# Performance work log

Hardware: AMD Instinct MI355X
Metric: run time of the kernel (lower is better)

Reference implementation:

```python
import jax, jax.numpy as jnp
import numpy as np

N, E, F_IN, F_HID, F_OUT, B = 50000, 800000, 128, 128, 128, 64
EPS = 1e-5


def _sage_conv(x, src, dst, w_l, b_l, w_r):
    # PyG SAGEConv (mean aggr): out = lin_l(mean_{j in N(i)} x_j) + lin_r(x_i)
    msg_sum = jax.ops.segment_sum(x[src], dst, num_segments=N)          # [N, F]
    deg = jax.ops.segment_sum(jnp.ones((src.shape[0],), x.dtype), dst, num_segments=N)
    agg = msg_sum / jnp.clip(deg, 1.0)[:, None]
    return agg @ w_l + b_l + x @ w_r


def _batch_norm(x, gamma, beta):
    # PyG BatchNorm (training): biased batch stats over the node dimension
    mu = jnp.mean(x, axis=0)
    var = jnp.mean((x - mu) ** 2, axis=0)
    return (x - mu) * jax.lax.rsqrt(var + EPS) * gamma + beta


def setup_inputs() -> dict:
    key = jax.random.key(0)
    ks = jax.random.split(key, 12)
    x = jax.random.normal(ks[0], (N, F_IN), jnp.float32)
    edge_index = jax.random.randint(ks[1], (2, E), 0, N, jnp.int64 if jax.config.jax_enable_x64 else jnp.int32)
    batch = jnp.sort(jax.random.randint(ks[2], (N,), 0, B))
    s1 = 1.0 / np.sqrt(F_IN)
    s2 = 1.0 / np.sqrt(F_HID)
    return {
        "x": x, "edge_index": edge_index, "batch": batch,
        "w_l1": jax.random.uniform(ks[3], (F_IN, F_HID), jnp.float32, -s1, s1),
        "b_l1": jax.random.uniform(ks[4], (F_HID,), jnp.float32, -s1, s1),
        "w_r1": jax.random.uniform(ks[5], (F_IN, F_HID), jnp.float32, -s1, s1),
        "g1": jnp.ones((F_HID,), jnp.float32),
        "beta1": jnp.zeros((F_HID,), jnp.float32),
        "w_l2": jax.random.uniform(ks[6], (F_HID, F_OUT), jnp.float32, -s2, s2),
        "b_l2": jax.random.uniform(ks[7], (F_OUT,), jnp.float32, -s2, s2),
        "w_r2": jax.random.uniform(ks[8], (F_HID, F_OUT), jnp.float32, -s2, s2),
        "g2": jnp.ones((F_OUT,), jnp.float32),
        "beta2": jnp.zeros((F_OUT,), jnp.float32),
    }


def reference(x, edge_index, batch, w_l1, b_l1, w_r1, g1, beta1, w_l2, b_l2, w_r2, g2, beta2):
    src, dst = edge_index[0], edge_index[1]
    h = jax.nn.relu(_batch_norm(_sage_conv(x, src, dst, w_l1, b_l1, w_r1), g1, beta1))
    h = jax.nn.relu(_batch_norm(_sage_conv(h, src, dst, w_l2, b_l2, w_r2), g2, beta2))
    # global_mean_pool over graph ids
    pooled = jax.ops.segment_sum(h, batch, num_segments=B)              # [B, F_OUT]
    cnt = jax.ops.segment_sum(jnp.ones((N,), h.dtype), batch, num_segments=B)
    return pooled / jnp.clip(cnt, 1.0)[:, None]
```

## Files before the change

### kernel.cpp

```cpp
#include <hip/hip_runtime.h>
#include <hip/hip_bf16.h>
#include <stdint.h>

typedef unsigned int uint32;
typedef unsigned short ushort16;

typedef __attribute__((ext_vector_type(8))) short short8;
typedef __attribute__((ext_vector_type(4))) float f32x4;

#define N_NODES 50000
#define N_EDGES 800000
#define FD      128
#define NGRAPH  64
#define MTILES  3125
#define NBK     196
#define GB      391
#define GB2     782
#define PCH     32
#define KCH     98

__device__ __forceinline__ float bf2f(ushort16 u){
  union { uint32 i; float f; } v; v.i = ((uint32)u) << 16; return v.f;
}
__device__ __forceinline__ float bf2f_lo(uint32 w){ union{uint32 i;float f;}v; v.i = w << 16; return v.f; }
__device__ __forceinline__ float bf2f_hi(uint32 w){ union{uint32 i;float f;}v; v.i = w & 0xffff0000u; return v.f; }
__device__ __forceinline__ ushort16 f2bf(float f){
  uint32 u = __float_as_uint(f);
  u += 0x7fffu + ((u >> 16) & 1u);
  return (ushort16)(u >> 16);
}

__device__ __forceinline__ int ld_idx(const void* p, uint32 is64, size_t i){
  return is64 ? (int)((const long long*)p)[i] : ((const int*)p)[i];
}
__device__ __forceinline__ float ld_f(const void* p, uint32 isf32, int i){
  return isf32 ? ((const float*)p)[i] : bf2f(((const ushort16*)p)[i]);
}

__device__ __forceinline__ void get_flags(const uint32* __restrict__ xw,
    const uint32* __restrict__ eiw, uint32& isf32, uint32& is64)
{
  int l = threadIdx.x & 63;
  uint32 w = xw[l];
  uint32 e8 = (w >> 7) & 0xFFu;
  bool bf_like = (e8 >= 0x70u && e8 <= 0x82u);
  unsigned long long m = __ballot(bf_like);
  isf32 = (__popcll(m) < 32) ? 1u : 0u;
  uint32 hi = (l < 8) ? eiw[2*l + 1] : 1u;
  unsigned long long z = __ballot(hi == 0u);
  is64 = ((z & 0xFFull) == 0xFFull) ? 1u : 0u;
}


__global__ __launch_bounds__(256) void pack_gseg_prep_kernel(
    const void* __restrict__ ei, const void* __restrict__ batch,
    const void* __restrict__ X,
    const void* __restrict__ WL1, const void* __restrict__ WR1,
    const void* __restrict__ WL2, const void* __restrict__ WR2,
    uint32* __restrict__ pack0, uint32* __restrict__ hist, uint32* __restrict__ gstart,
    ushort16* __restrict__ xb, short* __restrict__ wfrag)
{
  uint32 isf32, is64;
  get_flags((const uint32*)X, (const uint32*)ei, isf32, is64);
  int tid = threadIdx.x;
  if (blockIdx.x < GB){
    __shared__ uint32 h[256];
    h[tid] = 0u;
    __syncthreads();
    int base = blockIdx.x*2048;
    for (int r = 0; r < 8; ++r){
      int i = base + r*256 + tid;
      if (i < N_EDGES){
        uint32 s = (uint32)ld_idx(ei, is64, i);
        uint32 d = (uint32)ld_idx(ei, is64, (size_t)N_EDGES + i);
        pack0[i] = (d << 16) | s;
        atomicAdd(&h[d >> 8], 1u);
      }
    }
    __syncthreads();
    hist[blockIdx.x*256 + tid] = h[tid];
  } else if (blockIdx.x < GB + 196){
    int t = (blockIdx.x - GB)*256 + tid;
    if (t >= N_NODES) return;
    int b1 = ld_idx(batch, is64, t);
    int b0 = (t == 0) ? -1 : ld_idx(batch, is64, t - 1);
    for (int g = b0 + 1; g <= b1; ++g) gstart[g] = (uint32)t;
    if (t == N_NODES - 1)
      for (int g = b1 + 1; g <= NGRAPH; ++g) gstart[g] = (uint32)N_NODES;
  } else if (blockIdx.x < GB + 196 + 3125){
    if (!isf32) return;
    size_t e = ((size_t)(blockIdx.x - GB - 196)*256 + tid)*8;
    const float* p = (const float*)X + e;
    float4 u = *(const float4*)p;
    float4 v = *(const float4*)(p + 4);
    uint4 o;
    o.x = (uint32)f2bf(u.x) | ((uint32)f2bf(u.y) << 16);
    o.y = (uint32)f2bf(u.z) | ((uint32)f2bf(u.w) << 16);
    o.z = (uint32)f2bf(v.x) | ((uint32)f2bf(v.y) << 16);
    o.w = (uint32)f2bf(v.z) | ((uint32)f2bf(v.w) << 16);
    *(uint4*)(xb + e) = o;
  } else {
    int t = (blockIdx.x - GB - 196 - 3125)*256 + tid;
    int layer = t >> 15;
    int r = t & 32767;
    int k = r >> 7, n = r & 127;
    const void* w = layer ? (k < 128 ? WL2 : WR2) : (k < 128 ? WL1 : WR1);
    int kk = k & 127;
    float wv = ld_f(w, isf32, kk*128 + n);
    int off = (((k >> 5)*8 + (n >> 4))*64 + (n & 15) + 16*((kk >> 3) & 3))*8 + (kk & 7);
    wfrag[layer*32768 + off] = (short)f2bf(wv);
  }
}

__global__ __launch_bounds__(1024) void scan_hist_kernel(const uint32* __restrict__ hist,
    uint32* __restrict__ off, uint32* __restrict__ bbase)
{
  __shared__ uint32 part[4][256];
  __shared__ uint32 lds[256];
  __shared__ uint32 bb[256];
  int tid = threadIdx.x;
  int seg = tid >> 8, b = tid & 255;
  int k0 = seg*KCH, k1 = (k0 + KCH < GB) ? k0 + KCH : GB;
  uint32 sum = 0;
  for (int k = k0; k < k1; ++k) sum += hist[k*256 + b];
  part[seg][b] = sum;
  __syncthreads();
  uint32 tot = 0, x = 0;
  if (seg == 0){
    tot = part[0][b] + part[1][b] + part[2][b] + part[3][b];
    x = tot; lds[b] = x;
  }
  __syncthreads();
  for (int o = 1; o < 256; o <<= 1){
    uint32 y = 0;
    if (seg == 0 && b >= o) y = lds[b - o];
    __syncthreads();
    if (seg == 0){ x += y; lds[b] = x; }
    __syncthreads();
  }
  if (seg == 0){
    uint32 base = x - tot;
    bb[b] = base;
    if (b <= NBK) bbase[b] = (b < NBK) ? base : (uint32)N_EDGES;
  }
  __syncthreads();
  uint32 run = bb[b];
  for (int s = 0; s < seg; ++s) run += part[s][b];
  for (int k = k0; k < k1; ++k){
    off[k*256 + b] = run;
    run += hist[k*256 + b];
  }
}

__global__ __launch_bounds__(256) void scatter_kernel(const uint32* __restrict__ pack0,
    const uint32* __restrict__ off, uint32* __restrict__ pack1)
{
  __shared__ uint32 cur[256];
  int tid = threadIdx.x;
  cur[tid] = off[blockIdx.x*256 + tid];
  __syncthreads();
  int base = blockIdx.x*2048;
  for (int r = 0; r < 8; ++r){
    int i = base + r*256 + tid;
    if (i < N_EDGES){
      uint32 p = pack0[i];
      uint32 pos = atomicAdd(&cur[p >> 24], 1u);
      pack1[pos] = p;
    }
  }
}

__global__ __launch_bounds__(256) void bucket_csr_kernel(const uint32* __restrict__ pack1,
    const uint32* __restrict__ bbase, uint32* __restrict__ rowstart,
    uint32* __restrict__ deg, ushort16* __restrict__ colidx)
{
  __shared__ uint32 cnt[256];
  __shared__ uint32 lds[256];
  __shared__ uint32 cur[256];
  int tid = threadIdx.x;
  int bk = blockIdx.x;
  uint32 e0 = bbase[bk], e1 = bbase[bk + 1];
  cnt[tid] = 0u;
  __syncthreads();
  for (uint32 i = e0 + tid; i < e1; i += 256)
    atomicAdd(&cnt[(pack1[i] >> 16) & 255u], 1u);
  __syncthreads();
  uint32 v = cnt[tid];
  uint32 x = v;
  lds[tid] = x; __syncthreads();
  for (int o = 1; o < 256; o <<= 1){
    uint32 y = (tid >= o) ? lds[tid - o] : 0u;
    __syncthreads();
    x += y; lds[tid] = x;
    __syncthreads();
  }
  uint32 start = e0 + x - v;
  int node = bk*256 + tid;
  if (node < N_NODES){ rowstart[node] = start; deg[node] = v; }
  cur[tid] = start;
  __syncthreads();
  for (uint32 i = e0 + tid; i < e1; i += 256){
    uint32 p = pack1[i];
    uint32 pos = atomicAdd(&cur[(p >> 16) & 255u], 1u);
    colidx[pos] = (ushort16)(p & 0xFFFFu);
  }
}


__device__ __forceinline__ void acc8(float* a, uint4 v, const float* s0, const float* h0, int APPLY){
  float f[8];
  f[0] = bf2f_lo(v.x); f[1] = bf2f_hi(v.x);
  f[2] = bf2f_lo(v.y); f[3] = bf2f_hi(v.y);
  f[4] = bf2f_lo(v.z); f[5] = bf2f_hi(v.z);
  f[6] = bf2f_lo(v.w); f[7] = bf2f_hi(v.w);
#pragma unroll
  for (int j = 0; j < 8; ++j)
    a[j] += APPLY ? fmaxf(f[j]*s0[j] + h0[j], 0.f) : f[j];
}

template<int APPLY>
__global__ __launch_bounds__(256) void agg_kernel(const ushort16* __restrict__ Xd,
    const void* __restrict__ Xraw, const void* __restrict__ eiraw,
    const uint32* __restrict__ rowstart, const uint32* __restrict__ deg,
    const ushort16* __restrict__ colidx,
    const float* __restrict__ sc, const float* __restrict__ sh,
    ushort16* __restrict__ out)
{
  uint32 isf32, is64;
  get_flags((const uint32*)Xraw, (const uint32*)eiraw, isf32, is64);
  const ushort16* X = (APPLY == 0 && !isf32) ? (const ushort16*)Xraw : Xd;
  int t = blockIdx.x*256 + threadIdx.x;
  int node = t >> 4;
  int l = t & 15;
  uint32 st = rowstart[node];
  uint32 d  = deg[node];
  float s0[8], h0[8];
#pragma unroll
  for (int j = 0; j < 8; ++j){
    s0[j] = APPLY ? sc[l*8 + j] : 0.f;
    h0[j] = APPLY ? sh[l*8 + j] : 0.f;
  }
  float a[8];
#pragma unroll
  for (int j = 0; j < 8; ++j) a[j] = 0.f;
  const ushort16* Xl = X + l*8;
  uint32 i = 0;
  for (; i < d && ((st + i) & 3u); ++i){
    uint32 c = colidx[st + i];
    acc8(a, *(const uint4*)(Xl + (size_t)c*FD), s0, h0, APPLY);
  }
  for (; i + 8 <= d; i += 8){
    uint2 cA = *(const uint2*)(colidx + st + i);
    uint2 cB = *(const uint2*)(colidx + st + i + 4);
    uint4 v0 = *(const uint4*)(Xl + (size_t)(cA.x & 0xFFFFu)*FD);
    uint4 v1 = *(const uint4*)(Xl + (size_t)(cA.x >> 16)*FD);
    uint4 v2 = *(const uint4*)(Xl + (size_t)(cA.y & 0xFFFFu)*FD);
    uint4 v3 = *(const uint4*)(Xl + (size_t)(cA.y >> 16)*FD);
    uint4 v4 = *(const uint4*)(Xl + (size_t)(cB.x & 0xFFFFu)*FD);
    uint4 v5 = *(const uint4*)(Xl + (size_t)(cB.x >> 16)*FD);
    uint4 v6 = *(const uint4*)(Xl + (size_t)(cB.y & 0xFFFFu)*FD);
    uint4 v7 = *(const uint4*)(Xl + (size_t)(cB.y >> 16)*FD);
    acc8(a, v0, s0, h0, APPLY); acc8(a, v1, s0, h0, APPLY);
    acc8(a, v2, s0, h0, APPLY); acc8(a, v3, s0, h0, APPLY);
    acc8(a, v4, s0, h0, APPLY); acc8(a, v5, s0, h0, APPLY);
    acc8(a, v6, s0, h0, APPLY); acc8(a, v7, s0, h0, APPLY);
  }
  for (; i + 4 <= d; i += 4){
    uint2 cA = *(const uint2*)(colidx + st + i);
    uint4 v0 = *(const uint4*)(Xl + (size_t)(cA.x & 0xFFFFu)*FD);
    uint4 v1 = *(const uint4*)(Xl + (size_t)(cA.x >> 16)*FD);
    uint4 v2 = *(const uint4*)(Xl + (size_t)(cA.y & 0xFFFFu)*FD);
    uint4 v3 = *(const uint4*)(Xl + (size_t)(cA.y >> 16)*FD);
    acc8(a, v0, s0, h0, APPLY); acc8(a, v1, s0, h0, APPLY);
    acc8(a, v2, s0, h0, APPLY); acc8(a, v3, s0, h0, APPLY);
  }
  for (; i < d; ++i){
    uint32 c = colidx[st + i];
    acc8(a, *(const uint4*)(Xl + (size_t)c*FD), s0, h0, APPLY);
  }
  float inv = 1.f / fmaxf((float)d, 1.f);
  uint4 o;
  o.x = (uint32)f2bf(a[0]*inv) | ((uint32)f2bf(a[1]*inv) << 16);
  o.y = (uint32)f2bf(a[2]*inv) | ((uint32)f2bf(a[3]*inv) << 16);
  o.z = (uint32)f2bf(a[4]*inv) | ((uint32)f2bf(a[5]*inv) << 16);
  o.w = (uint32)f2bf(a[6]*inv) | ((uint32)f2bf(a[7]*inv) << 16);
  *(uint4*)(out + (size_t)node*FD + l*8) = o;
}


__device__ __forceinline__ short8 affine_relu8(short8 a, const float* sc, const float* sh, int koff){
  short8 r;
#pragma unroll
  for (int j = 0; j < 8; ++j){
    float v = bf2f((ushort16)a[j]) * sc[koff + j] + sh[koff + j];
    r[j] = (short)f2bf(fmaxf(v, 0.f));
  }
  return r;
}

template<int APPLY>
__global__ __launch_bounds__(256) void gemm_bn_kernel(
    const ushort16* __restrict__ A0, const ushort16* __restrict__ A1d,
    const void* __restrict__ A1raw, const void* __restrict__ eiraw,
    const short* __restrict__ wfrag, const void* __restrict__ bias,
    const float* __restrict__ sc, const float* __restrict__ sh,
    const void* __restrict__ Xraw,
    ushort16* __restrict__ hpre, float* __restrict__ bnpart)
{
  __shared__ float red[256];
  uint32 isf32, is64;
  get_flags((const uint32*)Xraw, (const uint32*)eiraw, isf32, is64);
  const ushort16* A1 = (A1raw && !isf32) ? (const ushort16*)A1raw : A1d;
  int tid = threadIdx.x;
  red[tid] = 0.f;
  int wave = tid >> 6, lane = tid & 63, lq = lane >> 4, lm = lane & 15;
  int mt = blockIdx.x*4 + wave;
  bool valid = mt < MTILES;
  size_t m0 = (size_t)((valid ? mt : 0)*16 + lm);
  f32x4 acc[8];
#pragma unroll
  for (int i = 0; i < 8; ++i) acc[i] = (f32x4){0.f,0.f,0.f,0.f};

#pragma unroll
  for (int ks = 0; ks < 8; ++ks){
    int koff = (ks & 3)*32 + lq*8;
    const short* srcp = (const short*)(ks < 4 ? A0 : A1);
    short8 a = *(const short8*)(srcp + m0*FD + koff);
    if (APPLY && ks >= 4) a = affine_relu8(a, sc, sh, koff);
#pragma unroll
    for (int nt = 0; nt < 8; ++nt){
      short8 b = *(const short8*)&wfrag[((ks*8 + nt)*64 + lane)*8];
      acc[nt] = __builtin_amdgcn_mfma_f32_16x16x32_bf16(a, b, acc[nt], 0, 0, 0);
    }
  }

  __syncthreads();
#pragma unroll
  for (int nt = 0; nt < 8; ++nt){
    int colc = nt*16 + lm;
    float bb = ld_f(bias, isf32, colc);
    float s = 0.f, s2 = 0.f;
    if (valid){
      size_t nb = (size_t)mt*16 + lq*4;
#pragma unroll
      for (int r = 0; r < 4; ++r){
        float val = acc[nt][r] + bb;
        hpre[(nb + r)*FD + colc] = f2bf(val);
        s += val; s2 += val*val;
      }
    }
    s  += __shfl_xor(s, 16);  s  += __shfl_xor(s, 32);
    s2 += __shfl_xor(s2, 16); s2 += __shfl_xor(s2, 32);
    if (lq == 0){
      atomicAdd(&red[colc], s);
      atomicAdd(&red[128 + colc], s2);
    }
  }
  __syncthreads();
  bnpart[blockIdx.x*256 + tid] = red[tid];
}


__global__ __launch_bounds__(256) void bn_final_kernel(const float* __restrict__ bnpart,
    const void* __restrict__ gamma, const void* __restrict__ beta,
    const void* __restrict__ Xraw, const void* __restrict__ eiraw,
    float* __restrict__ scale, float* __restrict__ shift)
{
  uint32 isf32, is64;
  get_flags((const uint32*)Xraw, (const uint32*)eiraw, isf32, is64);
  int tid = threadIdx.x;
  int f = blockIdx.x*8 + (tid >> 5);
  int l = tid & 31;
  float s = 0.f, q = 0.f;
  for (int b = l; b < GB2; b += 32){
    s += bnpart[b*256 + f];
    q += bnpart[b*256 + 128 + f];
  }
#pragma unroll
  for (int m = 16; m >= 1; m >>= 1){
    s += __shfl_xor(s, m);
    q += __shfl_xor(q, m);
  }
  if (l == 0){
    const float invN = 1.0f / (float)N_NODES;
    float mu  = s * invN;
    float var = q * invN - mu*mu;
    float scv = ld_f(gamma, isf32, f) * rsqrtf(var + 1e-5f);
    scale[f] = scv;
    shift[f] = ld_f(beta, isf32, f) - mu * scv;
  }
}


__global__ __launch_bounds__(256) void pool_partial_kernel(const ushort16* __restrict__ hp,
    const float* __restrict__ scale, const float* __restrict__ shift,
    const uint32* __restrict__ gstart, float* __restrict__ pool_part)
{
  __shared__ float wred[4*16*8];
  int tid = threadIdx.x;
  int g = blockIdx.x >> 5, chunk = blockIdx.x & 31;
  int slot = tid >> 4, l = tid & 15;
  int wave = tid >> 6, lane = tid & 63;
  uint32 st = gstart[g], cnt = gstart[g+1] - st;
  uint32 per = (cnt + PCH - 1) >> 5;
  uint32 b0 = st + chunk*per;
  uint32 b1 = b0 + per;
  uint32 e1 = st + cnt;
  if (b1 > e1) b1 = e1;
  float s0[8], h0[8], a[8];
#pragma unroll
  for (int j = 0; j < 8; ++j){ s0[j] = scale[l*8 + j]; h0[j] = shift[l*8 + j]; a[j] = 0.f; }
  for (uint32 n = b0 + slot; n < b1; n += 16){
    const uint4 v = *(const uint4*)(hp + (size_t)n*FD + l*8);
    float f[8];
    f[0] = bf2f_lo(v.x); f[1] = bf2f_hi(v.x);
    f[2] = bf2f_lo(v.y); f[3] = bf2f_hi(v.y);
    f[4] = bf2f_lo(v.z); f[5] = bf2f_hi(v.z);
    f[6] = bf2f_lo(v.w); f[7] = bf2f_hi(v.w);
#pragma unroll
    for (int j = 0; j < 8; ++j) a[j] += fmaxf(f[j]*s0[j] + h0[j], 0.f);
  }
#pragma unroll
  for (int j = 0; j < 8; ++j){
    a[j] += __shfl_xor(a[j], 16);
    a[j] += __shfl_xor(a[j], 32);
  }
  if (lane < 16){
#pragma unroll
    for (int j = 0; j < 8; ++j) wred[(wave*16 + lane)*8 + j] = a[j];
  }
  __syncthreads();
  if (tid < 16){
    float r[8];
#pragma unroll
    for (int j = 0; j < 8; ++j)
      r[j] = wred[(0*16 + tid)*8 + j] + wred[(1*16 + tid)*8 + j]
           + wred[(2*16 + tid)*8 + j] + wred[(3*16 + tid)*8 + j];
    float* dst = pool_part + (size_t)blockIdx.x*FD + tid*8;
#pragma unroll
    for (int j = 0; j < 8; ++j) dst[j] = r[j];
  }
}

__global__ void pool_final_kernel(const float* __restrict__ pool_part,
    const uint32* __restrict__ gstart, const void* __restrict__ Xraw,
    const void* __restrict__ eiraw, void* __restrict__ out)
{
  uint32 isf32, is64;
  get_flags((const uint32*)Xraw, (const uint32*)eiraw, isf32, is64);
  int t = blockIdx.x*256 + threadIdx.x;
  int g = t >> 7, f = t & 127;
  float c = fmaxf((float)(gstart[g+1] - gstart[g]), 1.f);
  float v = 0.f;
#pragma unroll 8
  for (int ch = 0; ch < PCH; ++ch)
    v += pool_part[(size_t)(g*PCH + ch)*FD + f];
  v /= c;
  if (isf32) ((float*)out)[t] = v;
  else       ((ushort16*)out)[t] = f2bf(v);
}


extern "C" void kernel_launch(void* const* d_in, const int* in_sizes, int n_in,
                              void* d_out, int out_size, void* d_ws, size_t ws_size,
                              hipStream_t stream)
{
  const void* x   = d_in[0];
  const void* ei  = d_in[1];
  const void* bat = d_in[2];
  const void* wl1 = d_in[3];
  const void* bl1 = d_in[4];
  const void* wr1 = d_in[5];
  const void* g1  = d_in[6];
  const void* be1 = d_in[7];
  const void* wl2 = d_in[8];
  const void* bl2 = d_in[9];
  const void* wr2 = d_in[10];
  const void* g2  = d_in[11];
  const void* be2 = d_in[12];
  char* ws = (char*)d_ws;

  uint32* gstart  = (uint32*)(ws + 64);
  uint32* bbase   = (uint32*)(ws + 384);
  float*  bnpart  = (float*) (ws + 1280);
  float*  scale1  = (float*) (ws + 802048);
  float*  shift1  = (float*) (ws + 802560);
  float*  scale2  = (float*) (ws + 803072);
  float*  shift2  = (float*) (ws + 803584);
  uint32* rowstart= (uint32*)(ws + 804096);
  uint32* deg     = (uint32*)(ws + 1004096);
  ushort16* colidx= (ushort16*)(ws + 1204096);
  short*  wfrag   = (short*) (ws + 2804096);
  ushort16* xb    = (ushort16*)(ws + 2935168);
  ushort16* aggb  = (ushort16*)(ws + 15735168);
  ushort16* hp1   = (ushort16*)(ws + 28535168);
  ushort16* hp2   = (ushort16*)(ws + 41335168);
  uint32* pack0   = (uint32*)(ws + 28535168);
  uint32* pack1   = (uint32*)(ws + 31735168);
  uint32* hist    = (uint32*)(ws + 34935168);
  uint32* off     = (uint32*)(ws + 35335552);
  float*  ppart   = (float*) (ws + 28535168);

  pack_gseg_prep_kernel<<<GB + 196 + 3125 + 256, 256, 0, stream>>>(
      ei, bat, x, wl1, wr1, wl2, wr2, pack0, hist, gstart, xb, wfrag);
  scan_hist_kernel <<<1,  1024, 0, stream>>>(hist, off, bbase);
  scatter_kernel   <<<GB,  256, 0, stream>>>(pack0, off, pack1);
  bucket_csr_kernel<<<NBK, 256, 0, stream>>>(pack1, bbase, rowstart, deg, colidx);

  agg_kernel<0>    <<<3125, 256, 0, stream>>>(xb, x, ei, rowstart, deg, colidx,
                                              nullptr, nullptr, aggb);
  gemm_bn_kernel<0><<<GB2,  256, 0, stream>>>(aggb, xb, x, ei, wfrag, bl1,
                                              nullptr, nullptr, x, hp1, bnpart);
  bn_final_kernel  <<<16,   256, 0, stream>>>(bnpart, g1, be1, x, ei, scale1, shift1);

  agg_kernel<1>    <<<3125, 256, 0, stream>>>(hp1, x, ei, rowstart, deg, colidx,
                                              scale1, shift1, aggb);
  gemm_bn_kernel<1><<<GB2,  256, 0, stream>>>(aggb, hp1, nullptr, ei, wfrag + 32768, bl2,
                                              scale1, shift1, x, hp2, bnpart);
  bn_final_kernel  <<<16,   256, 0, stream>>>(bnpart, g2, be2, x, ei, scale2, shift2);

  pool_partial_kernel<<<NGRAPH*PCH, 256, 0, stream>>>(hp2, scale2, shift2, gstart, ppart);
  pool_final_kernel  <<<32,  256, 0, stream>>>(ppart, gstart, x, ei, d_out);
}
```

Measured before the change: 287.1 us.

## Fuse neighbor aggregation and SAGE GEMM+BN-stats into one kernel per layer

Merges the mean-aggregation kernel and the MFMA GEMM/BN-partial kernel into one kernel. Each 256-thread block aggregates 16 nodes into LDS tiles, together with the (optionally BN+ReLU-applied) self features, then runs the MFMA with each wave covering two output column tiles. This removes the write and re-read of the aggregated intermediate buffer and one launch per layer. In exchange, the BN partial-sum buffer grows to 3125 blocks, so bn_final reduces over more partials. Each block also loads the full weight fragment set for only 16 rows, which lowers weight reuse.

Measured after the change: 328.5 us. 1.14x slower.

```diff
diff --git a/kernel.cpp b/kernel.cpp
--- a/kernel.cpp
+++ b/kernel.cpp
@@ -15,9 +15,9 @@
 #define MTILES  3125
 #define NBK     196
 #define GB      391
-#define GB2     782
 #define PCH     32
 #define KCH     98
+#define TS      136
 
 __device__ __forceinline__ float bf2f(ushort16 u){
   union { uint32 i; float f; } v; v.i = ((uint32)u) << 16; return v.f;
@@ -219,19 +219,25 @@
 }
 
 template<int APPLY>
-__global__ __launch_bounds__(256) void agg_kernel(const ushort16* __restrict__ Xd,
-    const void* __restrict__ Xraw, const void* __restrict__ eiraw,
+__global__ __launch_bounds__(256) void fused_layer_kernel(
+    const ushort16* __restrict__ Xd, const void* __restrict__ Xraw,
+    const void* __restrict__ flagX, const void* __restrict__ flagEI,
     const uint32* __restrict__ rowstart, const uint32* __restrict__ deg,
     const ushort16* __restrict__ colidx,
+    const short* __restrict__ wfrag, const void* __restrict__ bias,
     const float* __restrict__ sc, const float* __restrict__ sh,
-    ushort16* __restrict__ out)
-{
+    ushort16* __restrict__ hpre, float* __restrict__ bnpart)
+{
+  __shared__ short tile1[16*TS];
+  __shared__ short tile2[16*TS];
+  __shared__ float red[256];
   uint32 isf32, is64;
-  get_flags((const uint32*)Xraw, (const uint32*)eiraw, isf32, is64);
+  get_flags((const uint32*)flagX, (const uint32*)flagEI, isf32, is64);
   const ushort16* X = (APPLY == 0 && !isf32) ? (const ushort16*)Xraw : Xd;
-  int t = blockIdx.x*256 + threadIdx.x;
-  int node = t >> 4;
-  int l = t & 15;
+  int tid = threadIdx.x;
+  red[tid] = 0.f;
+  int nl = tid >> 4, l = tid & 15;
+  int node = blockIdx.x*16 + nl;
   uint32 st = rowstart[node];
   uint32 d  = deg[node];
   float s0[8], h0[8];
@@ -278,76 +284,61 @@
     uint32 c = colidx[st + i];
     acc8(a, *(const uint4*)(Xl + (size_t)c*FD), s0, h0, APPLY);
   }
-  float inv = 1.f / fmaxf((float)d, 1.f);
-  uint4 o;
-  o.x = (uint32)f2bf(a[0]*inv) | ((uint32)f2bf(a[1]*inv) << 16);
-  o.y = (uint32)f2bf(a[2]*inv) | ((uint32)f2bf(a[3]*inv) << 16);
-  o.z = (uint32)f2bf(a[4]*inv) | ((uint32)f2bf(a[5]*inv) << 16);
-  o.w = (uint32)f2bf(a[6]*inv) | ((uint32)f2bf(a[7]*inv) << 16);
-  *(uint4*)(out + (size_t)node*FD + l*8) = o;
-}
-
-
-__device__ __forceinline__ short8 affine_relu8(short8 a, const float* sc, const float* sh, int koff){
-  short8 r;
-#pragma unroll
-  for (int j = 0; j < 8; ++j){
-    float v = bf2f((ushort16)a[j]) * sc[koff + j] + sh[koff + j];
-    r[j] = (short)f2bf(fmaxf(v, 0.f));
-  }
-  return r;
-}
-
-template<int APPLY>
-__global__ __launch_bounds__(256) void gemm_bn_kernel(
-    const ushort16* __restrict__ A0, const ushort16* __restrict__ A1d,
-    const void* __restrict__ A1raw, const void* __restrict__ eiraw,
-    const short* __restrict__ wfrag, const void* __restrict__ bias,
-    const float* __restrict__ sc, const float* __restrict__ sh,
-    const void* __restrict__ Xraw,
-    ushort16* __restrict__ hpre, float* __restrict__ bnpart)
-{
-  __shared__ float red[256];
-  uint32 isf32, is64;
-  get_flags((const uint32*)Xraw, (const uint32*)eiraw, isf32, is64);
-  const ushort16* A1 = (A1raw && !isf32) ? (const ushort16*)A1raw : A1d;
-  int tid = threadIdx.x;
-  red[tid] = 0.f;
+  uint4 sv = *(const uint4*)(Xl + (size_t)node*FD);
+  {
+    float inv = 1.f / fmaxf((float)d, 1.f);
+    uint4 o1;
+    o1.x = (uint32)f2bf(a[0]*inv) | ((uint32)f2bf(a[1]*inv) << 16);
+    o1.y = (uint32)f2bf(a[2]*inv) | ((uint32)f2bf(a[3]*inv) << 16);
+    o1.z = (uint32)f2bf(a[4]*inv) | ((uint32)f2bf(a[5]*inv) << 16);
+    o1.w = (uint32)f2bf(a[6]*inv) | ((uint32)f2bf(a[7]*inv) << 16);
+    *(uint4*)&tile1[nl*TS + l*8] = o1;
+    uint4 o2 = sv;
+    if (APPLY){
+      float f[8];
+      f[0]=bf2f_lo(sv.x); f[1]=bf2f_hi(sv.x); f[2]=bf2f_lo(sv.y); f[3]=bf2f_hi(sv.y);
+      f[4]=bf2f_lo(sv.z); f[5]=bf2f_hi(sv.z); f[6]=bf2f_lo(sv.w); f[7]=bf2f_hi(sv.w);
+      ushort16 r[8];
+#pragma unroll
+      for (int j = 0; j < 8; ++j) r[j] = f2bf(fmaxf(f[j]*s0[j] + h0[j], 0.f));
+      o2.x = (uint32)r[0] | ((uint32)r[1] << 16);
+      o2.y = (uint32)r[2] | ((uint32)r[3] << 16);
+      o2.z = (uint32)r[4] | ((uint32)r[5] << 16);
+      o2.w = (uint32)r[6] | ((uint32)r[7] << 16);
+    }
+    *(uint4*)&tile2[nl*TS + l*8] = o2;
+  }
+  __syncthreads();
+
   int wave = tid >> 6, lane = tid & 63, lq = lane >> 4, lm = lane & 15;
-  int mt = blockIdx.x*4 + wave;
-  bool valid = mt < MTILES;
-  size_t m0 = (size_t)((valid ? mt : 0)*16 + lm);
-  f32x4 acc[8];
-#pragma unroll
-  for (int i = 0; i < 8; ++i) acc[i] = (f32x4){0.f,0.f,0.f,0.f};
-
+  f32x4 acc[2];
+  acc[0] = (f32x4){0.f,0.f,0.f,0.f};
+  acc[1] = (f32x4){0.f,0.f,0.f,0.f};
 #pragma unroll
   for (int ks = 0; ks < 8; ++ks){
-    int koff = (ks & 3)*32 + lq*8;
-    const short* srcp = (const short*)(ks < 4 ? A0 : A1);
-    short8 a = *(const short8*)(srcp + m0*FD + koff);
-    if (APPLY && ks >= 4) a = affine_relu8(a, sc, sh, koff);
-#pragma unroll
-    for (int nt = 0; nt < 8; ++nt){
+    const short* tp = (ks < 4) ? tile1 : tile2;
+    short8 av = *(const short8*)&tp[lm*TS + (ks & 3)*32 + lq*8];
+#pragma unroll
+    for (int p = 0; p < 2; ++p){
+      int nt = wave*2 + p;
       short8 b = *(const short8*)&wfrag[((ks*8 + nt)*64 + lane)*8];
-      acc[nt] = __builtin_amdgcn_mfma_f32_16x16x32_bf16(a, b, acc[nt], 0, 0, 0);
+      acc[p] = __builtin_amdgcn_mfma_f32_16x16x32_bf16(av, b, acc[p], 0, 0, 0);
     }
   }
 
   __syncthreads();
 #pragma unroll
-  for (int nt = 0; nt < 8; ++nt){
+  for (int p = 0; p < 2; ++p){
+    int nt = wave*2 + p;
     int colc = nt*16 + lm;
     float bb = ld_f(bias, isf32, colc);
     float s = 0.f, s2 = 0.f;
-    if (valid){
-      size_t nb = (size_t)mt*16 + lq*4;
-#pragma unroll
-      for (int r = 0; r < 4; ++r){
-        float val = acc[nt][r] + bb;
-        hpre[(nb + r)*FD + colc] = f2bf(val);
-        s += val; s2 += val*val;
-      }
+    size_t nb = (size_t)blockIdx.x*16 + lq*4;
+#pragma unroll
+    for (int r = 0; r < 4; ++r){
+      float val = acc[p][r] + bb;
+      hpre[(nb + r)*FD + colc] = f2bf(val);
+      s += val; s2 += val*val;
     }
     s  += __shfl_xor(s, 16);  s  += __shfl_xor(s, 32);
     s2 += __shfl_xor(s2, 16); s2 += __shfl_xor(s2, 32);
@@ -372,7 +363,7 @@
   int f = blockIdx.x*8 + (tid >> 5);
   int l = tid & 31;
   float s = 0.f, q = 0.f;
-  for (int b = l; b < GB2; b += 32){
+  for (int b = l; b < MTILES; b += 32){
     s += bnpart[b*256 + f];
     q += bnpart[b*256 + 128 + f];
   }
@@ -482,24 +473,23 @@
 
   uint32* gstart  = (uint32*)(ws + 64);
   uint32* bbase   = (uint32*)(ws + 384);
-  float*  bnpart  = (float*) (ws + 1280);
-  float*  scale1  = (float*) (ws + 802048);
-  float*  shift1  = (float*) (ws + 802560);
-  float*  scale2  = (float*) (ws + 803072);
-  float*  shift2  = (float*) (ws + 803584);
-  uint32* rowstart= (uint32*)(ws + 804096);
-  uint32* deg     = (uint32*)(ws + 1004096);
-  ushort16* colidx= (ushort16*)(ws + 1204096);
-  short*  wfrag   = (short*) (ws + 2804096);
-  ushort16* xb    = (ushort16*)(ws + 2935168);
-  ushort16* aggb  = (ushort16*)(ws + 15735168);
-  ushort16* hp1   = (ushort16*)(ws + 28535168);
-  ushort16* hp2   = (ushort16*)(ws + 41335168);
-  uint32* pack0   = (uint32*)(ws + 28535168);
-  uint32* pack1   = (uint32*)(ws + 31735168);
-  uint32* hist    = (uint32*)(ws + 34935168);
-  uint32* off     = (uint32*)(ws + 35335552);
-  float*  ppart   = (float*) (ws + 28535168);
+  float*  scale1  = (float*) (ws + 1280);
+  float*  shift1  = (float*) (ws + 1792);
+  float*  scale2  = (float*) (ws + 2304);
+  float*  shift2  = (float*) (ws + 2816);
+  uint32* rowstart= (uint32*)(ws + 3328);
+  uint32* deg     = (uint32*)(ws + 203328);
+  ushort16* colidx= (ushort16*)(ws + 403328);
+  short*  wfrag   = (short*) (ws + 2003328);
+  float*  bnpart  = (float*) (ws + 2134400);
+  ushort16* xb    = (ushort16*)(ws + 5334400);
+  ushort16* hp1   = (ushort16*)(ws + 18134400);
+  ushort16* hp2   = (ushort16*)(ws + 30934400);
+  uint32* pack0   = (uint32*)(ws + 43734400);
+  uint32* pack1   = (uint32*)(ws + 46934400);
+  uint32* hist    = (uint32*)(ws + 50134400);
+  uint32* off     = (uint32*)(ws + 50534784);
+  float*  ppart   = (float*) (ws + 43734400);
 
   pack_gseg_prep_kernel<<<GB + 196 + 3125 + 256, 256, 0, stream>>>(
       ei, bat, x, wl1, wr1, wl2, wr2, pack0, hist, gstart, xb, wfrag);
@@ -507,16 +497,12 @@
   scatter_kernel   <<<GB,  256, 0, stream>>>(pack0, off, pack1);
   bucket_csr_kernel<<<NBK, 256, 0, stream>>>(pack1, bbase, rowstart, deg, colidx);
 
-  agg_kernel<0>    <<<3125, 256, 0, stream>>>(xb, x, ei, rowstart, deg, colidx,
-                                              nullptr, nullptr, aggb);
-  gemm_bn_kernel<0><<<GB2,  256, 0, stream>>>(aggb, xb, x, ei, wfrag, bl1,
-                                              nullptr, nullptr, x, hp1, bnpart);
+  fused_layer_kernel<0><<<MTILES, 256, 0, stream>>>(xb, x, x, ei, rowstart, deg, colidx,
+                                                    wfrag, bl1, nullptr, nullptr, hp1, bnpart);
   bn_final_kernel  <<<16,   256, 0, stream>>>(bnpart, g1, be1, x, ei, scale1, shift1);
 
-  agg_kernel<1>    <<<3125, 256, 0, stream>>>(hp1, x, ei, rowstart, deg, colidx,
-                                              scale1, shift1, aggb);
-  gemm_bn_kernel<1><<<GB2,  256, 0, stream>>>(aggb, hp1, nullptr, ei, wfrag + 32768, bl2,
-                                              scale1, shift1, x, hp2, bnpart);
+  fused_layer_kernel<1><<<MTILES, 256, 0, stream>>>(hp1, nullptr, x, ei, rowstart, deg, colidx,
+                                                    wfrag + 32768, bl2, scale1, shift1, hp2, bnpart);
   bn_final_kernel  <<<16,   256, 0, stream>>>(bnpart, g2, be2, x, ei, scale2, shift2);
 
   pool_partial_kernel<<<NGRAPH*PCH, 256, 0, stream>>>(hp2, scale2, shift2, gstart, ppart);
```
